# Kernel optimization log

Hardware: AMD Instinct MI355X
Metric: run time of the kernel (lower is better)

## Reference

```python
import jax, jax.numpy as jnp
import numpy as np

NUM_HEADS = 4
NUM_GROUPS = 8
EPS = 1e-5


def setup_inputs() -> dict:
    key = jax.random.key(0)
    ks = jax.random.split(key, 4)
    B, C, H, W = 4, 256, 64, 64
    x = jax.random.normal(ks[0], (B, C, H, W), dtype=jnp.float32)
    norm_w = jnp.ones((C,), dtype=jnp.float32)
    norm_b = jnp.zeros((C,), dtype=jnp.float32)
    qkv_w = jax.random.normal(ks[1], (3 * C, C), dtype=jnp.float32) * (1.0 / np.sqrt(C))
    qkv_b = jnp.zeros((3 * C,), dtype=jnp.float32)
    proj_w = jax.random.normal(ks[2], (C, C), dtype=jnp.float32) * (1.0 / np.sqrt(C))
    proj_b = jnp.zeros((C,), dtype=jnp.float32)
    return {"x": x, "norm_w": norm_w, "norm_b": norm_b, "qkv_w": qkv_w,
            "qkv_b": qkv_b, "proj_w": proj_w, "proj_b": proj_b}


def _group_norm(x, w, b):
    B, C, H, W = x.shape
    g = x.reshape(B, NUM_GROUPS, C // NUM_GROUPS, H, W)
    mean = g.mean(axis=(2, 3, 4), keepdims=True)
    var = g.var(axis=(2, 3, 4), keepdims=True)
    g = (g - mean) * jax.lax.rsqrt(var + EPS)
    g = g.reshape(B, C, H, W)
    return g * w[None, :, None, None] + b[None, :, None, None]


def reference(x, norm_w, norm_b, qkv_w, qkv_b, proj_w, proj_b):
    B, C, H, W = x.shape
    hd = C // NUM_HEADS
    scale = hd ** (-0.5)
    h = _group_norm(x, norm_w, norm_b)
    # 1x1 conv == channel matmul: [3C,C] x [B,C,H,W]
    qkv = jnp.einsum('oc,bchw->bohw', qkv_w, h) + qkv_b[None, :, None, None]
    q, k, v = jnp.split(qkv, 3, axis=1)
    N = H * W
    q = q.reshape(B, NUM_HEADS, hd, N)
    k = k.reshape(B, NUM_HEADS, hd, N)
    v = v.reshape(B, NUM_HEADS, hd, N)
    attn = jnp.einsum('bhdn,bhdm->bhnm', q, k) * scale
    attn = jax.nn.softmax(attn, axis=-1)
    out = jnp.einsum('bhnm,bhdm->bhdn', attn, v)
    out = out.reshape(B, C, H, W)
    proj = jnp.einsum('oc,bchw->bohw', proj_w, out) + proj_b[None, :, None, None]
    return x + proj
```

## Files before the change

### kernel.cpp

```cpp
#include <hip/hip_runtime.h>

#define BATCH 4
#define CCH   256
#define NSP   4096
#define GRPSZ (32 * 4096)
#define NHEAD 4
#define HD    64

typedef __attribute__((ext_vector_type(8))) short short8;
typedef __attribute__((ext_vector_type(8))) unsigned short ushort8_t;
typedef __attribute__((ext_vector_type(4))) float f32x4;

__device__ __forceinline__ unsigned short f2b(float f) {
    unsigned u = __builtin_bit_cast(unsigned, f);
    unsigned r = u + 0x7FFFu + ((u >> 16) & 1u);
    return (unsigned short)(r >> 16);
}

__global__ __launch_bounds__(256) void gn_partial(const float* __restrict__ x,
                                                  float* __restrict__ sums) {
    int chunk = blockIdx.x & 7;
    int bg    = blockIdx.x >> 3;
    const float* base = x + (size_t)bg * GRPSZ + (size_t)chunk * (GRPSZ / 8);
    int t = threadIdx.x;
    float s = 0.f, ss = 0.f;
#pragma unroll
    for (int i = 0; i < 16; ++i) {
        float4 v = *(const float4*)&base[(t + i * 256) * 4];
        s  += v.x + v.y + v.z + v.w;
        ss += v.x * v.x + v.y * v.y + v.z * v.z + v.w * v.w;
    }
    __shared__ float rs[256], rss[256];
    rs[t] = s; rss[t] = ss;
    __syncthreads();
    for (int off = 128; off > 0; off >>= 1) {
        if (t < off) { rs[t] += rs[t + off]; rss[t] += rss[t + off]; }
        __syncthreads();
    }
    if (t == 0) {
        sums[blockIdx.x * 2]     = rs[0];
        sums[blockIdx.x * 2 + 1] = rss[0];
    }
}

__global__ __launch_bounds__(256) void gn_pack(const float* __restrict__ x,
                                               const float* __restrict__ sums,
                                               const float* __restrict__ gw,
                                               const float* __restrict__ gb,
                                               unsigned short* __restrict__ hT) {
    __shared__ float LT[64][65];
    __shared__ float wcs[64], bcs[64];
    int b = blockIdx.z, c0 = blockIdx.y * 64, n0 = blockIdx.x * 64;
    int t = threadIdx.x;
    if (t < 64) {
        int c  = c0 + t;
        int bg = b * 8 + (c >> 5);
        float s = 0.f, ss = 0.f;
#pragma unroll
        for (int i = 0; i < 8; ++i) {
            s  += sums[(bg * 8 + i) * 2];
            ss += sums[(bg * 8 + i) * 2 + 1];
        }
        const float invn = 1.f / (float)GRPSZ;
        float mean = s * invn;
        float var  = ss * invn - mean * mean;
        float inv  = rsqrtf(var + 1e-5f);
        float wc = gw[c] * inv;
        wcs[t] = wc;
        bcs[t] = gb[c] - mean * wc;
    }
    __syncthreads();
    int cl4 = (t & 15) * 4, cr = t >> 4;
#pragma unroll
    for (int p = 0; p < 4; ++p) {
        int c = cr + p * 16;
        float4 v = *(const float4*)&x[(size_t)(b * 256 + c0 + c) * 4096 + n0 + cl4];
        float wc = wcs[c], bb = bcs[c];
        LT[c][cl4 + 0] = v.x * wc + bb;
        LT[c][cl4 + 1] = v.y * wc + bb;
        LT[c][cl4 + 2] = v.z * wc + bb;
        LT[c][cl4 + 3] = v.w * wc + bb;
    }
    __syncthreads();
#pragma unroll
    for (int p = 0; p < 2; ++p) {
        int n  = (t >> 3) + p * 32;
        int c8 = (t & 7) * 8;
        ushort8_t w;
#pragma unroll
        for (int i = 0; i < 8; ++i) w[i] = f2b(LT[c8 + i][n]);
        *(ushort8_t*)&hT[((size_t)b * 4096 + n0 + n) * 256 + c0 + c8] = w;
    }
}

__global__ __launch_bounds__(256) void gemm_qkv(const float* __restrict__ W,
                                                const unsigned short* __restrict__ hT,
                                                const float* __restrict__ bias,
                                                unsigned short* __restrict__ Qbf,
                                                unsigned short* __restrict__ Ktbf,
                                                unsigned short* __restrict__ Vbf) {
    __shared__ unsigned short Wl[64 * 64];
    __shared__ unsigned short Hl[64 * 64];
    int b = blockIdx.z, o0 = blockIdx.y * 64, n0 = blockIdx.x * 64;
    int t = threadIdx.x, lane = t & 63, wid = t >> 6, g = lane >> 4, cl = lane & 15;
    f32x4 acc[4];
#pragma unroll
    for (int j = 0; j < 4; ++j) acc[j] = (f32x4){0.f, 0.f, 0.f, 0.f};
    int sr = t >> 2;
    int sk = (t & 3) * 16;
    int swr = (sr & 7) << 3;
    int swa = (cl & 7) << 3;
    for (int k0 = 0; k0 < 256; k0 += 64) {
        __syncthreads();
        {
            const float* wr = &W[(size_t)(o0 + sr) * 256 + k0 + sk];
            float4 w0 = *(const float4*)&wr[0],  w1 = *(const float4*)&wr[4];
            float4 w2 = *(const float4*)&wr[8],  w3 = *(const float4*)&wr[12];
            ushort8_t u0 = {f2b(w0.x), f2b(w0.y), f2b(w0.z), f2b(w0.w),
                            f2b(w1.x), f2b(w1.y), f2b(w1.z), f2b(w1.w)};
            ushort8_t u1 = {f2b(w2.x), f2b(w2.y), f2b(w2.z), f2b(w2.w),
                            f2b(w3.x), f2b(w3.y), f2b(w3.z), f2b(w3.w)};
            *(ushort8_t*)&Wl[sr * 64 + (sk ^ swr)]       = u0;
            *(ushort8_t*)&Wl[sr * 64 + ((sk + 8) ^ swr)] = u1;
        }
        {
            const ushort8_t* hr = (const ushort8_t*)&hT[((size_t)b * 4096 + n0 + sr) * 256 + k0 + sk];
            *(ushort8_t*)&Hl[sr * 64 + (sk ^ swr)]       = hr[0];
            *(ushort8_t*)&Hl[sr * 64 + ((sk + 8) ^ swr)] = hr[1];
        }
        __syncthreads();
#pragma unroll
        for (int ks = 0; ks < 2; ++ks) {
            short8 a = *(short8*)&Hl[(wid * 16 + cl) * 64 + ((ks * 32 + g * 8) ^ swa)];
#pragma unroll
            for (int j = 0; j < 4; ++j) {
                short8 bb = *(short8*)&Wl[(j * 16 + cl) * 64 + ((ks * 32 + g * 8) ^ swa)];
                acc[j] = __builtin_amdgcn_mfma_f32_16x16x32_bf16(a, bb, acc[j], 0, 0, 0);
            }
        }
    }
    int sect = blockIdx.y >> 2, head = blockIdx.y & 3;
    size_t tilebase = (((size_t)b * NHEAD + head) * 64 + blockIdx.x) * 4096;
    int nrow = wid * 16 + g * 4;
    if (sect == 0) {
#pragma unroll
        for (int j = 0; j < 4; ++j) {
            float bi = bias[o0 + j * 16 + cl];
#pragma unroll
            for (int r = 0; r < 4; ++r)
                Qbf[tilebase + (size_t)(nrow + r) * 64 + j * 16 + cl] =
                    f2b((acc[j][r] + bi) * 0.125f);
        }
    } else if (sect == 1) {
#pragma unroll
        for (int j = 0; j < 4; ++j) {
            float bi = bias[o0 + j * 16 + cl];
#pragma unroll
            for (int r = 0; r < 4; ++r) {
                int key = nrow + r;
                int sw  = ((key ^ (key >> 3)) & 7) << 3;
                Ktbf[tilebase + (size_t)key * 64 + ((j * 16 + cl) ^ sw)] =
                    f2b(acc[j][r] + bi);
            }
        }
    } else {
        __syncthreads();
        unsigned short* VL = Wl;
#pragma unroll
        for (int j = 0; j < 4; ++j) {
            float bi = bias[o0 + j * 16 + cl];
            int d = j * 16 + cl;
#pragma unroll
            for (int r = 0; r < 4; ++r) {
                int key = nrow + r;
                VL[d * 64 + (key ^ ((d & 7) << 3))] = f2b(acc[j][r] + bi);
            }
        }
        __syncthreads();
        ushort8_t* dst = (ushort8_t*)&Vbf[tilebase];
        const ushort8_t* srcl = (const ushort8_t*)VL;
        dst[t]       = srcl[t];
        dst[t + 256] = srcl[t + 256];
    }
}

__global__ __launch_bounds__(256) void gemm_proj(const float* __restrict__ W,
                                                 const unsigned short* __restrict__ aT,
                                                 const float* __restrict__ bias,
                                                 const float* __restrict__ x,
                                                 float* __restrict__ Out) {
    __shared__ unsigned short Wl[64 * 64];
    __shared__ unsigned short Al[64 * 64];
    int b = blockIdx.z, o0 = blockIdx.y * 64, n0 = blockIdx.x * 64;
    int t = threadIdx.x, lane = t & 63, wid = t >> 6, g = lane >> 4, cl = lane & 15;
    f32x4 acc[4];
#pragma unroll
    for (int j = 0; j < 4; ++j) acc[j] = (f32x4){0.f, 0.f, 0.f, 0.f};
    int sr = t >> 2, sk = (t & 3) * 16;
    int swr = (sr & 7) << 3;
    int swa = (cl & 7) << 3;
    for (int k0 = 0; k0 < 256; k0 += 64) {
        __syncthreads();
        {
            const float* wr = &W[(size_t)(o0 + sr) * 256 + k0 + sk];
            float4 w0 = *(const float4*)&wr[0],  w1 = *(const float4*)&wr[4];
            float4 w2 = *(const float4*)&wr[8],  w3 = *(const float4*)&wr[12];
            ushort8_t u0 = {f2b(w0.x), f2b(w0.y), f2b(w0.z), f2b(w0.w),
                            f2b(w1.x), f2b(w1.y), f2b(w1.z), f2b(w1.w)};
            ushort8_t u1 = {f2b(w2.x), f2b(w2.y), f2b(w2.z), f2b(w2.w),
                            f2b(w3.x), f2b(w3.y), f2b(w3.z), f2b(w3.w)};
            *(ushort8_t*)&Wl[sr * 64 + (sk ^ swr)]       = u0;
            *(ushort8_t*)&Wl[sr * 64 + ((sk + 8) ^ swr)] = u1;
        }
        {
            const ushort8_t* ar = (const ushort8_t*)&aT[((size_t)b * 4096 + n0 + sr) * 256 + k0 + sk];
            *(ushort8_t*)&Al[sr * 64 + (sk ^ swr)]       = ar[0];
            *(ushort8_t*)&Al[sr * 64 + ((sk + 8) ^ swr)] = ar[1];
        }
        __syncthreads();
#pragma unroll
        for (int ks = 0; ks < 2; ++ks) {
            short8 a = *(short8*)&Wl[(wid * 16 + cl) * 64 + ((ks * 32 + g * 8) ^ swa)];
#pragma unroll
            for (int j = 0; j < 4; ++j) {
                short8 bb = *(short8*)&Al[(j * 16 + cl) * 64 + ((ks * 32 + g * 8) ^ swa)];
                acc[j] = __builtin_amdgcn_mfma_f32_16x16x32_bf16(a, bb, acc[j], 0, 0, 0);
            }
        }
    }
    float bi[4];
#pragma unroll
    for (int r = 0; r < 4; ++r) bi[r] = bias[o0 + wid * 16 + g * 4 + r];
#pragma unroll
    for (int r = 0; r < 4; ++r) {
        int o = o0 + wid * 16 + g * 4 + r;
        size_t rowbase = ((size_t)b * 256 + o) * 4096 + n0;
#pragma unroll
        for (int j = 0; j < 4; ++j) {
            size_t idx = rowbase + j * 16 + cl;
            Out[idx] = acc[j][r] + bi[r] + x[idx];
        }
    }
}

__global__ __launch_bounds__(256, 4) void flash_mfma(const unsigned short* __restrict__ Qbf,
                                                     const unsigned short* __restrict__ Ktbf,
                                                     const unsigned short* __restrict__ Vbf,
                                                     unsigned short* __restrict__ aoutbf) {
    __shared__ char smem[24576];
    unsigned short* Kt = (unsigned short*)smem;
    unsigned short* Vs = (unsigned short*)(smem + 8192);
    unsigned short* Pb = (unsigned short*)(smem + 16384);

    const int t    = threadIdx.x;
    const int lane = t & 63;
    const int wid  = t >> 6;
    const int g    = lane >> 4;
    const int cl   = lane & 15;

    const int head = blockIdx.y, b = blockIdx.z;
    const int bh   = b * NHEAD + head;

    const unsigned short* Qt = Qbf + (((size_t)bh * 64 + blockIdx.x) * 4096);
    short8 qf[2];
    qf[0] = *(const short8*)&Qt[(wid * 16 + cl) * 64 + g * 8];
    qf[1] = *(const short8*)&Qt[(wid * 16 + cl) * 64 + 32 + g * 8];

    f32x4 o_acc[4];
#pragma unroll
    for (int ds = 0; ds < 4; ++ds) o_acc[ds] = (f32x4){0.f, 0.f, 0.f, 0.f};
    float m[4], l[4];
#pragma unroll
    for (int r = 0; r < 4; ++r) { m[r] = -1e30f; l[r] = 0.f; }

    for (int tile = 0; tile < 64; ++tile) {
        __syncthreads();
        {
            const ushort8_t* kg = (const ushort8_t*)(Ktbf + (((size_t)bh * 64 + tile) * 4096));
            const ushort8_t* vg = (const ushort8_t*)(Vbf  + (((size_t)bh * 64 + tile) * 4096));
            ushort8_t* kl = (ushort8_t*)Kt;
            ushort8_t* vl = (ushort8_t*)Vs;
            kl[t]       = kg[t];
            kl[t + 256] = kg[t + 256];
            vl[t]       = vg[t];
            vl[t + 256] = vg[t + 256];
        }
        __syncthreads();

        f32x4 accs[4];
#pragma unroll
        for (int s = 0; s < 4; ++s) {
            f32x4 a = (f32x4){0.f, 0.f, 0.f, 0.f};
            int row = s * 16 + cl;
            int sw  = ((row ^ (row >> 3)) & 7) << 3;
#pragma unroll
            for (int h = 0; h < 2; ++h) {
                short8 kf = *(short8*)&Kt[row * 64 + ((h * 32 + g * 8) ^ sw)];
                a = __builtin_amdgcn_mfma_f32_16x16x32_bf16(qf[h], kf, a, 0, 0, 0);
            }
            accs[s] = a;
        }

        unsigned short pb16[4][4];
#pragma unroll
        for (int r = 0; r < 4; ++r) {
            float rm = fmaxf(fmaxf(accs[0][r], accs[1][r]), fmaxf(accs[2][r], accs[3][r]));
#pragma unroll
            for (int mask = 1; mask < 16; mask <<= 1)
                rm = fmaxf(rm, __shfl_xor(rm, mask));
            float mn   = fmaxf(m[r], rm);
            float corr = __expf(m[r] - mn);
            m[r] = mn;
            l[r] *= corr;
            o_acc[0][r] *= corr; o_acc[1][r] *= corr;
            o_acc[2][r] *= corr; o_acc[3][r] *= corr;
            float ps = 0.f;
#pragma unroll
            for (int s = 0; s < 4; ++s) {
                float p = __expf(accs[s][r] - mn);
                ps += p;
                pb16[r][s] = f2b(p);
            }
            l[r] += ps;
        }

        unsigned short* Pw = Pb + wid * 16 * 64;
#pragma unroll
        for (int r = 0; r < 4; ++r) {
            int row = g * 4 + r;
#pragma unroll
            for (int s = 0; s < 4; ++s) {
                int col = s * 16 + cl;
                Pw[row * 64 + (col ^ ((row & 7) << 3))] = pb16[r][s];
            }
        }
        short8 pf[2];
#pragma unroll
        for (int h2 = 0; h2 < 2; ++h2)
            pf[h2] = *(short8*)&Pw[cl * 64 + ((h2 * 32 + g * 8) ^ ((cl & 7) << 3))];
#pragma unroll
        for (int ds = 0; ds < 4; ++ds) {
            int vrow = ds * 16 + cl;
#pragma unroll
            for (int h2 = 0; h2 < 2; ++h2) {
                short8 vf = *(short8*)&Vs[vrow * 64 + ((h2 * 32 + g * 8) ^ ((cl & 7) << 3))];
                o_acc[ds] = __builtin_amdgcn_mfma_f32_16x16x32_bf16(pf[h2], vf, o_acc[ds], 0, 0, 0);
            }
        }
    }

    float inv[4];
#pragma unroll
    for (int r = 0; r < 4; ++r) {
        float s = l[r];
#pragma unroll
        for (int mask = 1; mask < 16; mask <<= 1) s += __shfl_xor(s, mask);
        inv[r] = 1.f / s;
    }
    unsigned short* Ab = aoutbf + ((size_t)b * 4096 + blockIdx.x * 64 + wid * 16) * 256 + head * 64;
#pragma unroll
    for (int ds = 0; ds < 4; ++ds)
#pragma unroll
        for (int r = 0; r < 4; ++r)
            Ab[(size_t)(g * 4 + r) * 256 + ds * 16 + cl] = f2b(o_acc[ds][r] * inv[r]);
}

extern "C" void kernel_launch(void* const* d_in, const int* in_sizes, int n_in,
                              void* d_out, int out_size, void* d_ws, size_t ws_size,
                              hipStream_t stream) {
    const float* x    = (const float*)d_in[0];
    const float* nw   = (const float*)d_in[1];
    const float* nb   = (const float*)d_in[2];
    const float* qkvw = (const float*)d_in[3];
    const float* qkvb = (const float*)d_in[4];
    const float* pw   = (const float*)d_in[5];
    const float* pb   = (const float*)d_in[6];
    float* out = (float*)d_out;

    char* ws = (char*)d_ws;
    float* sums = (float*)ws;
    unsigned short* hT     = (unsigned short*)(ws + (1 << 16));
    unsigned short* Qbf    = hT     + (size_t)BATCH * NSP * CCH;
    unsigned short* Ktbf   = Qbf    + (size_t)BATCH * NHEAD * NSP * HD;
    unsigned short* Vbf    = Ktbf   + (size_t)BATCH * NHEAD * NSP * HD;
    unsigned short* aoutbf = Vbf    + (size_t)BATCH * NHEAD * NSP * HD;

    gn_partial<<<dim3(256), dim3(256), 0, stream>>>(x, sums);
    gn_pack<<<dim3(64, 4, BATCH), dim3(256), 0, stream>>>(x, sums, nw, nb, hT);
    gemm_qkv<<<dim3(64, 12, BATCH), dim3(256), 0, stream>>>(qkvw, hT, qkvb, Qbf, Ktbf, Vbf);
    flash_mfma<<<dim3(64, NHEAD, BATCH), dim3(256), 0, stream>>>(Qbf, Ktbf, Vbf, aoutbf);
    gemm_proj<<<dim3(64, 4, BATCH), dim3(256), 0, stream>>>(pw, aoutbf, pb, x, out);
}
```

Baseline: 292.4 us.

## Double-buffer K/V tiles in flash attention and use exp2 with lazy rescaling

```diff
diff --git a/kernel.cpp b/kernel.cpp
--- a/kernel.cpp
+++ b/kernel.cpp
@@ -1,4 +1,5 @@
 #include <hip/hip_runtime.h>
+#include <hip/hip_bf16.h>
 
 #define BATCH 4
 #define CCH   256
@@ -15,6 +16,13 @@
     unsigned u = __builtin_bit_cast(unsigned, f);
     unsigned r = u + 0x7FFFu + ((u >> 16) & 1u);
     return (unsigned short)(r >> 16);
+}
+__device__ __forceinline__ unsigned short b16p(float f) {
+    __hip_bfloat16 h = __float2bfloat16(f);
+    return __builtin_bit_cast(unsigned short, h);
+}
+__device__ __forceinline__ float ex2(float x) {
+    float r; asm("v_exp_f32 %0, %1" : "=v"(r) : "v"(x)); return r;
 }
 
 __global__ __launch_bounds__(256) void gn_partial(const float* __restrict__ x,
@@ -143,13 +151,14 @@
     size_t tilebase = (((size_t)b * NHEAD + head) * 64 + blockIdx.x) * 4096;
     int nrow = wid * 16 + g * 4;
     if (sect == 0) {
+        const float qsc = 0.18033688011112042f;
 #pragma unroll
         for (int j = 0; j < 4; ++j) {
             float bi = bias[o0 + j * 16 + cl];
 #pragma unroll
             for (int r = 0; r < 4; ++r)
                 Qbf[tilebase + (size_t)(nrow + r) * 64 + j * 16 + cl] =
-                    f2b((acc[j][r] + bi) * 0.125f);
+                    f2b((acc[j][r] + bi) * qsc);
         }
     } else if (sect == 1) {
 #pragma unroll
@@ -247,10 +256,9 @@
                                                      const unsigned short* __restrict__ Ktbf,
                                                      const unsigned short* __restrict__ Vbf,
                                                      unsigned short* __restrict__ aoutbf) {
-    __shared__ char smem[24576];
-    unsigned short* Kt = (unsigned short*)smem;
-    unsigned short* Vs = (unsigned short*)(smem + 8192);
-    unsigned short* Pb = (unsigned short*)(smem + 16384);
+    __shared__ unsigned short Kbuf[2][4096];
+    __shared__ unsigned short Vbuf[2][4096];
+    __shared__ unsigned short Pbuf[4096];
 
     const int t    = threadIdx.x;
     const int lane = t & 63;
@@ -266,6 +274,9 @@
     qf[0] = *(const short8*)&Qt[(wid * 16 + cl) * 64 + g * 8];
     qf[1] = *(const short8*)&Qt[(wid * 16 + cl) * 64 + 32 + g * 8];
 
+    const ushort8_t* kg = (const ushort8_t*)(Ktbf + (size_t)bh * 64 * 4096);
+    const ushort8_t* vg = (const ushort8_t*)(Vbf  + (size_t)bh * 64 * 4096);
+
     f32x4 o_acc[4];
 #pragma unroll
     for (int ds = 0; ds < 4; ++ds) o_acc[ds] = (f32x4){0.f, 0.f, 0.f, 0.f};
@@ -273,19 +284,22 @@
 #pragma unroll
     for (int r = 0; r < 4; ++r) { m[r] = -1e30f; l[r] = 0.f; }
 
+    ushort8_t kr0 = kg[t], kr1 = kg[t + 256];
+    ushort8_t vr0 = vg[t], vr1 = vg[t + 256];
+    ((ushort8_t*)&Kbuf[0][0])[t] = kr0;  ((ushort8_t*)&Kbuf[0][0])[t + 256] = kr1;
+    ((ushort8_t*)&Vbuf[0][0])[t] = vr0;  ((ushort8_t*)&Vbuf[0][0])[t + 256] = vr1;
+    __syncthreads();
+
     for (int tile = 0; tile < 64; ++tile) {
-        __syncthreads();
-        {
-            const ushort8_t* kg = (const ushort8_t*)(Ktbf + (((size_t)bh * 64 + tile) * 4096));
-            const ushort8_t* vg = (const ushort8_t*)(Vbf  + (((size_t)bh * 64 + tile) * 4096));
-            ushort8_t* kl = (ushort8_t*)Kt;
-            ushort8_t* vl = (ushort8_t*)Vs;
-            kl[t]       = kg[t];
-            kl[t + 256] = kg[t + 256];
-            vl[t]       = vg[t];
-            vl[t + 256] = vg[t + 256];
-        }
-        __syncthreads();
+        const int cur = tile & 1;
+        const unsigned short* KT = &Kbuf[cur][0];
+        const unsigned short* VS = &Vbuf[cur][0];
+        if (tile < 63) {
+            const ushort8_t* kn = kg + (size_t)(tile + 1) * 512;
+            const ushort8_t* vn = vg + (size_t)(tile + 1) * 512;
+            kr0 = kn[t]; kr1 = kn[t + 256];
+            vr0 = vn[t]; vr1 = vn[t + 256];
+        }
 
         f32x4 accs[4];
 #pragma unroll
@@ -295,36 +309,47 @@
             int sw  = ((row ^ (row >> 3)) & 7) << 3;
 #pragma unroll
             for (int h = 0; h < 2; ++h) {
-                short8 kf = *(short8*)&Kt[row * 64 + ((h * 32 + g * 8) ^ sw)];
+                short8 kf = *(const short8*)&KT[row * 64 + ((h * 32 + g * 8) ^ sw)];
                 a = __builtin_amdgcn_mfma_f32_16x16x32_bf16(qf[h], kf, a, 0, 0, 0);
             }
             accs[s] = a;
         }
 
-        unsigned short pb16[4][4];
+        float nm[4];
+        int need = 0;
 #pragma unroll
         for (int r = 0; r < 4; ++r) {
             float rm = fmaxf(fmaxf(accs[0][r], accs[1][r]), fmaxf(accs[2][r], accs[3][r]));
 #pragma unroll
             for (int mask = 1; mask < 16; mask <<= 1)
                 rm = fmaxf(rm, __shfl_xor(rm, mask));
-            float mn   = fmaxf(m[r], rm);
-            float corr = __expf(m[r] - mn);
-            m[r] = mn;
-            l[r] *= corr;
-            o_acc[0][r] *= corr; o_acc[1][r] *= corr;
-            o_acc[2][r] *= corr; o_acc[3][r] *= corr;
+            nm[r] = fmaxf(m[r], rm);
+            need |= (rm > m[r] + 8.f) ? 1 : 0;
+        }
+        if (__any(need)) {
+#pragma unroll
+            for (int r = 0; r < 4; ++r) {
+                float corr = ex2(m[r] - nm[r]);
+                l[r] *= corr;
+                o_acc[0][r] *= corr; o_acc[1][r] *= corr;
+                o_acc[2][r] *= corr; o_acc[3][r] *= corr;
+                m[r] = nm[r];
+            }
+        }
+        unsigned short pb16[4][4];
+#pragma unroll
+        for (int r = 0; r < 4; ++r) {
             float ps = 0.f;
 #pragma unroll
             for (int s = 0; s < 4; ++s) {
-                float p = __expf(accs[s][r] - mn);
+                float p = ex2(accs[s][r] - m[r]);
                 ps += p;
-                pb16[r][s] = f2b(p);
+                pb16[r][s] = b16p(p);
             }
             l[r] += ps;
         }
 
-        unsigned short* Pw = Pb + wid * 16 * 64;
+        unsigned short* Pw = &Pbuf[wid * 16 * 64];
 #pragma unroll
         for (int r = 0; r < 4; ++r) {
             int row = g * 4 + r;
@@ -337,16 +362,24 @@
         short8 pf[2];
 #pragma unroll
         for (int h2 = 0; h2 < 2; ++h2)
-            pf[h2] = *(short8*)&Pw[cl * 64 + ((h2 * 32 + g * 8) ^ ((cl & 7) << 3))];
+            pf[h2] = *(const short8*)&Pw[cl * 64 + ((h2 * 32 + g * 8) ^ ((cl & 7) << 3))];
 #pragma unroll
         for (int ds = 0; ds < 4; ++ds) {
             int vrow = ds * 16 + cl;
 #pragma unroll
             for (int h2 = 0; h2 < 2; ++h2) {
-                short8 vf = *(short8*)&Vs[vrow * 64 + ((h2 * 32 + g * 8) ^ ((cl & 7) << 3))];
+                short8 vf = *(const short8*)&VS[vrow * 64 + ((h2 * 32 + g * 8) ^ ((cl & 7) << 3))];
                 o_acc[ds] = __builtin_amdgcn_mfma_f32_16x16x32_bf16(pf[h2], vf, o_acc[ds], 0, 0, 0);
             }
         }
+
+        if (tile < 63) {
+            ushort8_t* KN = (ushort8_t*)&Kbuf[cur ^ 1][0];
+            ushort8_t* VN = (ushort8_t*)&Vbuf[cur ^ 1][0];
+            KN[t] = kr0;  KN[t + 256] = kr1;
+            VN[t] = vr0;  VN[t + 256] = vr1;
+        }
+        __syncthreads();
     }
 
     float inv[4];
```

After: 279.2 us. 1.05x faster.
